# Performance work log

Hardware: AMD Instinct MI355X
Metric: run time of the kernel (lower is better)

The kernel has to match this reference:

```python
import jax, jax.numpy as jnp
import numpy as np

B, S, NT, D, NU = 1024, 200, 10000, 256, 100000
BETA_1 = 0.1


def setup_inputs() -> dict:
    key = jax.random.key(0)
    ks = jax.random.split(key, 6)
    user_id = jax.random.randint(ks[0], (B,), 0, NU)
    event_type = jax.random.randint(ks[1], (B, S), 0, NT + 1)  # 0 = pad
    adjacent_matrix = jax.random.uniform(ks[2], (NT, NT), dtype=jnp.float32)
    pop_encoding = jax.random.normal(ks[3], (NT + 1, D), dtype=jnp.float32)
    event_emb = jax.random.normal(ks[4], (NT + 1, D), dtype=jnp.float32) * 0.02
    user_emb = jax.random.normal(ks[5], (NU, D), dtype=jnp.float32) * 0.02
    return dict(user_id=user_id, event_type=event_type,
                adjacent_matrix=adjacent_matrix, pop_encoding=pop_encoding,
                evaluation=0, event_emb=event_emb, user_emb=user_emb)


def _l2norm(x, eps):
    # tf.nn.l2_normalize: x * rsqrt(max(sum(x^2), eps))
    return x * jax.lax.rsqrt(jnp.maximum(jnp.sum(x * x, axis=-1, keepdims=True), eps))


def reference(user_id, event_type, adjacent_matrix, pop_encoding, evaluation, event_emb, user_emb):
    non_pad = (event_type != 0).astype(jnp.float32)[..., None]          # [B,S,1]
    enc = event_emb[event_type]                                          # [B,S,D]
    usr = user_emb[user_id]                                              # [B,D]
    pop = pop_encoding[event_type] * non_pad                             # [B,S,D]
    # enc += sign(enc) * l2_normalize(user_output) (default eps 1e-12)
    enc = enc + jnp.sign(enc) * _l2norm(usr, 1e-12)[:, None, :]
    # per-sample adjacency: two-axis gather of the item-item matrix
    idx = jnp.where(event_type > 0, event_type - 1, 0)                   # [B,S]
    adj = adjacent_matrix[idx[:, :, None], idx[:, None, :]]              # [B,S,S]
    has_valid = (jnp.sum(event_type > 0, axis=1) > 0).astype(jnp.float32)
    adj = adj * has_valid[:, None, None]  # rows with all-pad stay zero, as in the loop
    output = jnp.mean(enc, axis=1)                                       # [B,D]
    user_embeddings = jnp.concatenate([output, jnp.mean(pop, axis=1) * BETA_1], axis=-1)  # [B,2D]
    if evaluation:
        item_encoding = event_emb[1:]                                    # [NT,D]
        scores = user_embeddings[:, :D] @ item_encoding.T
    else:
        item_encoding = jnp.concatenate([event_emb[1:], pop_encoding[1:] * BETA_1], axis=-1)  # [NT,2D]
        scores = user_embeddings @ item_encoding.T                       # [B,NT]
    prediction = jnp.tanh(_l2norm(scores, 1e-05))
    return prediction, user_embeddings, pop, adj
```

## Files before the change

### kernel.cpp

```cpp
#include <hip/hip_runtime.h>
#include <math.h>

#define NB 1024
#define NS 200
#define NTOK 10000
#define ND 256
#define BETA 0.1f

static constexpr size_t PRED_OFF = 0;
static constexpr size_t UE_OFF   = (size_t)NB * NTOK;
static constexpr size_t POP_OFF  = UE_OFF + (size_t)NB * 2 * ND;
static constexpr size_t ADJ_OFF  = POP_OFF + (size_t)NB * NS * ND;

static constexpr size_t WS_SIDX   = 0;
static constexpr size_t WS_HV     = WS_SIDX + (size_t)NB * NS;
static constexpr size_t WS_COUNTS = WS_HV + NB;
static constexpr size_t WS_OFFS   = WS_COUNTS + NTOK;
static constexpr size_t WS_CURSOR = WS_OFFS + NTOK + 1;
static constexpr size_t WS_PAIRS  = WS_CURSOR + NTOK;

__global__ __launch_bounds__(256) void k_embed(
    const int* __restrict__ user_id,
    const int* __restrict__ event_type,
    const float* __restrict__ pop_encoding,
    const float* __restrict__ event_emb,
    const float* __restrict__ user_emb,
    float* __restrict__ ue,
    float* __restrict__ pop)
{
    const int b = blockIdx.x;
    const int d = threadIdx.x;

    const int uid = user_id[b];
    const float u = user_emb[(size_t)uid * ND + d];

    float ss = u * u;
    #pragma unroll
    for (int o = 32; o > 0; o >>= 1) ss += __shfl_down(ss, o, 64);
    __shared__ float wss[4];
    const int wid = d >> 6, lane = d & 63;
    if (lane == 0) wss[wid] = ss;
    __syncthreads();
    const float tot = wss[0] + wss[1] + wss[2] + wss[3];
    const float nu = u * rsqrtf(fmaxf(tot, 1e-12f));

    __shared__ int et_s[NS];
    if (d < NS) et_s[d] = event_type[(size_t)b * NS + d];
    __syncthreads();

    float acc = 0.f, pacc = 0.f;
    #pragma unroll 4
    for (int s = 0; s < NS; ++s) {
        const int et = et_s[s];
        const float e = event_emb[(size_t)et * ND + d];
        const float sg = (e > 0.f) ? 1.f : ((e < 0.f) ? -1.f : 0.f);
        acc += e + sg * nu;
        float p = pop_encoding[(size_t)et * ND + d];
        p = (et != 0) ? p : 0.f;
        pacc += p;
        __builtin_nontemporal_store(p, &pop[((size_t)b * NS + s) * ND + d]);
    }
    ue[(size_t)b * (2 * ND) + d]      = acc * (1.f / NS);
    ue[(size_t)b * (2 * ND) + ND + d] = pacc * (1.f / NS) * BETA;
}

__global__ __launch_bounds__(256) void k_zero(int* __restrict__ counts)
{
    const int i = blockIdx.x * 256 + threadIdx.x;
    if (i < NTOK) counts[i] = 0;
}

__global__ __launch_bounds__(256) void k_prep(
    const int* __restrict__ event_type,
    int* __restrict__ sidx_all,
    float* __restrict__ hvf,
    int* __restrict__ counts)
{
    const int b = blockIdx.x;
    const int t = threadIdx.x;
    __shared__ int hv_s;
    if (t == 0) hv_s = 0;
    __syncthreads();
    if (t < NS) {
        const int et = event_type[(size_t)b * NS + t];
        const int r  = (et > 0) ? (et - 1) : 0;
        sidx_all[(size_t)b * NS + t] = r;
        if (et > 0) hv_s = 1;
        atomicAdd(&counts[r], 1);
    }
    __syncthreads();
    if (t == 0) hvf[b] = hv_s ? 1.f : 0.f;
}

#define SCAN_CHUNK 40
__global__ __launch_bounds__(256) void k_scan(
    const int* __restrict__ counts,
    int* __restrict__ offsets,
    int* __restrict__ cursor)
{
    const int t = threadIdx.x;
    int sum = 0;
    int local[SCAN_CHUNK];
    #pragma unroll
    for (int k = 0; k < SCAN_CHUNK; ++k) {
        const int idx = t * SCAN_CHUNK + k;
        const int c = (idx < NTOK) ? counts[idx] : 0;
        local[k] = c;
        sum += c;
    }
    __shared__ int part[256];
    part[t] = sum;
    __syncthreads();
    for (int o = 1; o < 256; o <<= 1) {
        const int v = (t >= o) ? part[t - o] : 0;
        __syncthreads();
        part[t] += v;
        __syncthreads();
    }
    int running = part[t] - sum;
    #pragma unroll
    for (int k = 0; k < SCAN_CHUNK; ++k) {
        const int idx = t * SCAN_CHUNK + k;
        if (idx < NTOK) {
            offsets[idx] = running;
            cursor[idx]  = running;
            running += local[k];
        }
    }
    if (t == 255) offsets[NTOK] = part[255];
}

__global__ __launch_bounds__(256) void k_scatter(
    const int* __restrict__ sidx_all,
    int* __restrict__ cursor,
    int* __restrict__ pairs)
{
    const int b = blockIdx.x;
    const int t = threadIdx.x;
    if (t < NS) {
        const int r = sidx_all[(size_t)b * NS + t];
        const int slot = atomicAdd(&cursor[r], 1);
        pairs[slot] = b * NS + t;
    }
}

__global__ __launch_bounds__(256) void k_adj2(
    const float* __restrict__ A,
    const int* __restrict__ sidx_all,
    const int* __restrict__ offsets,
    const int* __restrict__ pairs,
    const float* __restrict__ hvf,
    float* __restrict__ adj)
{
    const int r = blockIdx.x;
    const int t = threadIdx.x;
    const int p0 = offsets[r];
    const int n  = offsets[r + 1] - p0;
    if (n == 0) return;

    __shared__ __align__(16) float rowlds[NTOK];
    const float4* Arow = (const float4*)(A + (size_t)r * NTOK);
    #pragma unroll 4
    for (int l = t; l < NTOK / 4; l += 256)
        ((float4*)rowlds)[l] = Arow[l];
    __syncthreads();

    const int n_el = n * NS;
    for (int l = t; l < n_el; l += 256) {
        const int pi = l / NS;
        const int j  = l - pi * NS;
        const int pv = pairs[p0 + pi];
        const int b  = pv / NS;
        const int c  = sidx_all[(size_t)b * NS + j];
        const float v = rowlds[c] * hvf[b];
        __builtin_nontemporal_store(v, &adj[(size_t)pv * NS + j]);
    }
}

typedef __attribute__((ext_vector_type(8))) short bf16x8;
typedef __attribute__((ext_vector_type(4))) float f32x4;

static __device__ inline unsigned short f2bf(float f) {
    unsigned int u = __float_as_uint(f);
    return (unsigned short)((u + 0x7fffu + ((u >> 16) & 1u)) >> 16);
}

#define GBM 128
#define GBN 128
#define GBK 32
#define LDK 40

__global__ __launch_bounds__(256) void k_gemm_mfma(
    const float* __restrict__ ue,
    const float* __restrict__ event_emb,
    const float* __restrict__ pop_encoding,
    float* __restrict__ scores)
{
    __shared__ __align__(16) unsigned short As[GBM * LDK];
    __shared__ __align__(16) unsigned short Bs[GBN * LDK];

    const int t  = threadIdx.x;
    const int bn = blockIdx.x, bm = blockIdx.y;
    const int m0 = bm * GBM, n0 = bn * GBN;

    const int wave = t >> 6, lane = t & 63;
    const int ww = wave & 1, wm = wave >> 1;
    const int lr = lane & 15;
    const int kg = lane >> 4;

    const int kq = t & 7;
    const int rq = t >> 3;

    f32x4 acc[4][4] = {};

    for (int k0 = 0; k0 < 512; k0 += GBK) {
        #pragma unroll
        for (int i = 0; i < 4; ++i) {
            const int r = rq + 32 * i;
            const float4 v = *(const float4*)&ue[(size_t)(m0 + r) * 512 + k0 + kq * 4];
            ushort4 h;
            h.x = f2bf(v.x); h.y = f2bf(v.y); h.z = f2bf(v.z); h.w = f2bf(v.w);
            *(ushort4*)&As[r * LDK + kq * 4] = h;
        }
        const bool loK = (k0 < 256);
        const float scale = loK ? 1.f : BETA;
        #pragma unroll
        for (int i = 0; i < 4; ++i) {
            const int r = rq + 32 * i;
            const int gn = n0 + r;
            ushort4 h = {0, 0, 0, 0};
            if (gn < NTOK) {
                const float* src = loK
                    ? &event_emb[(size_t)(gn + 1) * ND + k0 + kq * 4]
                    : &pop_encoding[(size_t)(gn + 1) * ND + (k0 - 256) + kq * 4];
                const float4 v = *(const float4*)src;
                h.x = f2bf(v.x * scale); h.y = f2bf(v.y * scale);
                h.z = f2bf(v.z * scale); h.w = f2bf(v.w * scale);
            }
            *(ushort4*)&Bs[r * LDK + kq * 4] = h;
        }
        __syncthreads();

        bf16x8 a[4], b[4];
        #pragma unroll
        for (int mf = 0; mf < 4; ++mf)
            a[mf] = *(const bf16x8*)&As[(wm * 64 + mf * 16 + lr) * LDK + kg * 8];
        #pragma unroll
        for (int nf = 0; nf < 4; ++nf)
            b[nf] = *(const bf16x8*)&Bs[(ww * 64 + nf * 16 + lr) * LDK + kg * 8];
        #pragma unroll
        for (int mf = 0; mf < 4; ++mf)
            #pragma unroll
            for (int nf = 0; nf < 4; ++nf)
                acc[mf][nf] = __builtin_amdgcn_mfma_f32_16x16x32_bf16(
                    a[mf], b[nf], acc[mf][nf], 0, 0, 0);
        __syncthreads();
    }

    #pragma unroll
    for (int mf = 0; mf < 4; ++mf) {
        const int row = m0 + wm * 64 + mf * 16 + kg * 4;
        #pragma unroll
        for (int nf = 0; nf < 4; ++nf) {
            const int col = n0 + ww * 64 + nf * 16 + lr;
            if (col < NTOK) {
                #pragma unroll
                for (int r = 0; r < 4; ++r)
                    scores[(size_t)(row + r) * NTOK + col] = acc[mf][nf][r];
            }
        }
    }
}

__global__ __launch_bounds__(256) void k_norm(float* __restrict__ scores)
{
    const int b = blockIdx.x;
    const int t = threadIdx.x;
    float* row = scores + (size_t)b * NTOK;

    float ss = 0.f;
    for (int n = t; n < NTOK; n += 256) {
        const float v = row[n];
        ss += v * v;
    }
    #pragma unroll
    for (int o = 32; o > 0; o >>= 1) ss += __shfl_down(ss, o, 64);
    __shared__ float wss[4];
    const int wid = t >> 6, lane = t & 63;
    if (lane == 0) wss[wid] = ss;
    __syncthreads();
    const float tot = wss[0] + wss[1] + wss[2] + wss[3];
    const float rs = rsqrtf(fmaxf(tot, 1e-5f));

    for (int n = t; n < NTOK; n += 256)
        row[n] = tanhf(row[n] * rs);
}

extern "C" void kernel_launch(void* const* d_in, const int* in_sizes, int n_in,
                              void* d_out, int out_size, void* d_ws, size_t ws_size,
                              hipStream_t stream) {
    const int*   user_id      = (const int*)d_in[0];
    const int*   event_type   = (const int*)d_in[1];
    const float* adjacent     = (const float*)d_in[2];
    const float* pop_encoding = (const float*)d_in[3];
    const float* event_emb    = (const float*)d_in[5];
    const float* user_emb     = (const float*)d_in[6];

    float* out  = (float*)d_out;
    float* pred = out + PRED_OFF;
    float* ue   = out + UE_OFF;
    float* pop  = out + POP_OFF;
    float* adj  = out + ADJ_OFF;

    int*   ws       = (int*)d_ws;
    int*   sidx_all = ws + WS_SIDX;
    float* hvf      = (float*)(ws + WS_HV);
    int*   counts   = ws + WS_COUNTS;
    int*   offsets  = ws + WS_OFFS;
    int*   cursor   = ws + WS_CURSOR;
    int*   pairs    = ws + WS_PAIRS;

    k_embed<<<NB, 256, 0, stream>>>(user_id, event_type, pop_encoding,
                                    event_emb, user_emb, ue, pop);

    k_zero<<<(NTOK + 255) / 256, 256, 0, stream>>>(counts);
    k_prep<<<NB, 256, 0, stream>>>(event_type, sidx_all, hvf, counts);
    k_scan<<<1, 256, 0, stream>>>(counts, offsets, cursor);
    k_scatter<<<NB, 256, 0, stream>>>(sidx_all, cursor, pairs);
    k_adj2<<<NTOK, 256, 0, stream>>>(adjacent, sidx_all, offsets, pairs, hvf, adj);

    dim3 ggrid((NTOK + GBN - 1) / GBN, NB / GBM);
    k_gemm_mfma<<<ggrid, 256, 0, stream>>>(ue, event_emb, pop_encoding, pred);
    k_norm<<<NB, 256, 0, stream>>>(pred);
}
```

Baseline: 385.7 us.

## Pre-convert GEMM operands to bf16 and vectorize embed, adjacency and norm kernels

Adds a pass that converts the item encoding (event_emb and scaled pop_encoding) to a packed bf16 matrix, and has k_embed also write a bf16 copy of the user embeddings. The GEMM can then load bf16 directly, with no fp32 loads or in-loop conversion. k_embed is rewritten so that each wave handles a quarter of the sequence with float4 loads and stores, followed by a shared-memory reduction. k_adj2 assigns one pair per wave with int4/float4 vectorized gathers and stores, and k_norm uses float4 accesses. The cost is an extra kernel launch and extra workspace traffic for the bf16 copies.

```diff
diff --git a/kernel.cpp b/kernel.cpp
--- a/kernel.cpp
+++ b/kernel.cpp
@@ -18,6 +18,16 @@
 static constexpr size_t WS_OFFS   = WS_COUNTS + NTOK;
 static constexpr size_t WS_CURSOR = WS_OFFS + NTOK + 1;
 static constexpr size_t WS_PAIRS  = WS_CURSOR + NTOK;
+static constexpr size_t WS_UEBF   = 440640;
+static constexpr size_t WS_IEBF   = WS_UEBF + 262144;
+
+typedef __attribute__((ext_vector_type(8))) short bf16x8;
+typedef __attribute__((ext_vector_type(4))) float f32x4;
+
+static __device__ inline unsigned short f2bf(float f) {
+    unsigned int u = __float_as_uint(f);
+    return (unsigned short)((u + 0x7fffu + ((u >> 16) & 1u)) >> 16);
+}
 
 __global__ __launch_bounds__(256) void k_embed(
     const int* __restrict__ user_id,
@@ -26,42 +36,86 @@
     const float* __restrict__ event_emb,
     const float* __restrict__ user_emb,
     float* __restrict__ ue,
+    unsigned short* __restrict__ ue_bf,
     float* __restrict__ pop)
 {
-    const int b = blockIdx.x;
-    const int d = threadIdx.x;
+    const int b  = blockIdx.x;
+    const int t  = threadIdx.x;
+    const int sg = t >> 6;
+    const int tl = t & 63;
 
     const int uid = user_id[b];
-    const float u = user_emb[(size_t)uid * ND + d];
-
-    float ss = u * u;
-    #pragma unroll
-    for (int o = 32; o > 0; o >>= 1) ss += __shfl_down(ss, o, 64);
-    __shared__ float wss[4];
-    const int wid = d >> 6, lane = d & 63;
-    if (lane == 0) wss[wid] = ss;
-    __syncthreads();
-    const float tot = wss[0] + wss[1] + wss[2] + wss[3];
-    const float nu = u * rsqrtf(fmaxf(tot, 1e-12f));
+    const float4 u4 = *(const float4*)&user_emb[(size_t)uid * ND + tl * 4];
+
+    float ss = u4.x * u4.x + u4.y * u4.y + u4.z * u4.z + u4.w * u4.w;
+    #pragma unroll
+    for (int o = 32; o > 0; o >>= 1) ss += __shfl_xor(ss, o, 64);
+    const float rn = rsqrtf(fmaxf(ss, 1e-12f));
+    const float4 nu4 = {u4.x * rn, u4.y * rn, u4.z * rn, u4.w * rn};
 
     __shared__ int et_s[NS];
-    if (d < NS) et_s[d] = event_type[(size_t)b * NS + d];
-    __syncthreads();
-
-    float acc = 0.f, pacc = 0.f;
-    #pragma unroll 4
-    for (int s = 0; s < NS; ++s) {
+    if (t < NS) et_s[t] = event_type[(size_t)b * NS + t];
+    __syncthreads();
+
+    float4 eacc = {0.f, 0.f, 0.f, 0.f};
+    float4 pacc = {0.f, 0.f, 0.f, 0.f};
+    #pragma unroll 2
+    for (int it = 0; it < NS / 4; ++it) {
+        const int s  = sg + 4 * it;
         const int et = et_s[s];
-        const float e = event_emb[(size_t)et * ND + d];
-        const float sg = (e > 0.f) ? 1.f : ((e < 0.f) ? -1.f : 0.f);
-        acc += e + sg * nu;
-        float p = pop_encoding[(size_t)et * ND + d];
-        p = (et != 0) ? p : 0.f;
-        pacc += p;
-        __builtin_nontemporal_store(p, &pop[((size_t)b * NS + s) * ND + d]);
-    }
-    ue[(size_t)b * (2 * ND) + d]      = acc * (1.f / NS);
-    ue[(size_t)b * (2 * ND) + ND + d] = pacc * (1.f / NS) * BETA;
+        const float4 e = *(const float4*)&event_emb[(size_t)et * ND + tl * 4];
+        float4 p = *(const float4*)&pop_encoding[(size_t)et * ND + tl * 4];
+        const float z = (et != 0) ? 1.f : 0.f;
+        p.x *= z; p.y *= z; p.z *= z; p.w *= z;
+        eacc.x += e.x + ((e.x > 0.f) ? nu4.x : ((e.x < 0.f) ? -nu4.x : 0.f));
+        eacc.y += e.y + ((e.y > 0.f) ? nu4.y : ((e.y < 0.f) ? -nu4.y : 0.f));
+        eacc.z += e.z + ((e.z > 0.f) ? nu4.z : ((e.z < 0.f) ? -nu4.z : 0.f));
+        eacc.w += e.w + ((e.w > 0.f) ? nu4.w : ((e.w < 0.f) ? -nu4.w : 0.f));
+        pacc.x += p.x; pacc.y += p.y; pacc.z += p.z; pacc.w += p.w;
+        const f32x4 pv = {p.x, p.y, p.z, p.w};
+        __builtin_nontemporal_store(pv, (f32x4*)&pop[((size_t)b * NS + s) * ND + tl * 4]);
+    }
+
+    __shared__ __align__(16) float4 es[4][64];
+    __shared__ __align__(16) float4 ps[4][64];
+    es[sg][tl] = eacc;
+    ps[sg][tl] = pacc;
+    __syncthreads();
+
+    if (t < 64) {
+        float4 ef = es[0][t], pf = ps[0][t];
+        #pragma unroll
+        for (int w = 1; w < 4; ++w) {
+            const float4 e2 = es[w][t], p2 = ps[w][t];
+            ef.x += e2.x; ef.y += e2.y; ef.z += e2.z; ef.w += e2.w;
+            pf.x += p2.x; pf.y += p2.y; pf.z += p2.z; pf.w += p2.w;
+        }
+        const float se = 1.f / NS, sp = BETA / NS;
+        const float4 eo = {ef.x * se, ef.y * se, ef.z * se, ef.w * se};
+        const float4 po = {pf.x * sp, pf.y * sp, pf.z * sp, pf.w * sp};
+        *(float4*)&ue[(size_t)b * 512 + t * 4]       = eo;
+        *(float4*)&ue[(size_t)b * 512 + 256 + t * 4] = po;
+        ushort4 he = {f2bf(eo.x), f2bf(eo.y), f2bf(eo.z), f2bf(eo.w)};
+        ushort4 hp = {f2bf(po.x), f2bf(po.y), f2bf(po.z), f2bf(po.w)};
+        *(ushort4*)&ue_bf[(size_t)b * 512 + t * 4]       = he;
+        *(ushort4*)&ue_bf[(size_t)b * 512 + 256 + t * 4] = hp;
+    }
+}
+
+__global__ __launch_bounds__(256) void k_iebf(
+    const float* __restrict__ ee,
+    const float* __restrict__ pe,
+    unsigned short* __restrict__ ie)
+{
+    const int idx = blockIdx.x * 256 + threadIdx.x;
+    if (idx >= NTOK * 128) return;
+    const int row = idx >> 7;
+    const int kq  = idx & 127;
+    float4 v; float sc;
+    if (kq < 64) { v = *(const float4*)&ee[(size_t)(row + 1) * ND + kq * 4]; sc = 1.f; }
+    else         { v = *(const float4*)&pe[(size_t)(row + 1) * ND + (kq - 64) * 4]; sc = BETA; }
+    ushort4 h = {f2bf(v.x * sc), f2bf(v.y * sc), f2bf(v.z * sc), f2bf(v.w * sc)};
+    *(ushort4*)&ie[(size_t)row * 512 + kq * 4] = h;
 }
 
 __global__ __launch_bounds__(256) void k_zero(int* __restrict__ counts)
@@ -165,24 +219,21 @@
         ((float4*)rowlds)[l] = Arow[l];
     __syncthreads();
 
-    const int n_el = n * NS;
-    for (int l = t; l < n_el; l += 256) {
-        const int pi = l / NS;
-        const int j  = l - pi * NS;
+    const int wave = t >> 6, lane = t & 63;
+    for (int pi = wave; pi < n; pi += 4) {
         const int pv = pairs[p0 + pi];
         const int b  = pv / NS;
-        const int c  = sidx_all[(size_t)b * NS + j];
-        const float v = rowlds[c] * hvf[b];
-        __builtin_nontemporal_store(v, &adj[(size_t)pv * NS + j]);
-    }
-}
-
-typedef __attribute__((ext_vector_type(8))) short bf16x8;
-typedef __attribute__((ext_vector_type(4))) float f32x4;
-
-static __device__ inline unsigned short f2bf(float f) {
-    unsigned int u = __float_as_uint(f);
-    return (unsigned short)((u + 0x7fffu + ((u >> 16) & 1u)) >> 16);
+        const float hv = hvf[b];
+        if (lane < 50) {
+            const int4 c4 = *(const int4*)&sidx_all[(size_t)b * NS + lane * 4];
+            f32x4 v;
+            v.x = rowlds[c4.x] * hv;
+            v.y = rowlds[c4.y] * hv;
+            v.z = rowlds[c4.z] * hv;
+            v.w = rowlds[c4.w] * hv;
+            __builtin_nontemporal_store(v, (f32x4*)&adj[(size_t)pv * NS + lane * 4]);
+        }
+    }
 }
 
 #define GBM 128
@@ -191,9 +242,8 @@
 #define LDK 40
 
 __global__ __launch_bounds__(256) void k_gemm_mfma(
-    const float* __restrict__ ue,
-    const float* __restrict__ event_emb,
-    const float* __restrict__ pop_encoding,
+    const unsigned short* __restrict__ ue_bf,
+    const unsigned short* __restrict__ ie_bf,
     float* __restrict__ scores)
 {
     __shared__ __align__(16) unsigned short As[GBM * LDK];
@@ -217,26 +267,16 @@
         #pragma unroll
         for (int i = 0; i < 4; ++i) {
             const int r = rq + 32 * i;
-            const float4 v = *(const float4*)&ue[(size_t)(m0 + r) * 512 + k0 + kq * 4];
-            ushort4 h;
-            h.x = f2bf(v.x); h.y = f2bf(v.y); h.z = f2bf(v.z); h.w = f2bf(v.w);
-            *(ushort4*)&As[r * LDK + kq * 4] = h;
-        }
-        const bool loK = (k0 < 256);
-        const float scale = loK ? 1.f : BETA;
+            *(ushort4*)&As[r * LDK + kq * 4] =
+                *(const ushort4*)&ue_bf[(size_t)(m0 + r) * 512 + k0 + kq * 4];
+        }
         #pragma unroll
         for (int i = 0; i < 4; ++i) {
             const int r = rq + 32 * i;
             const int gn = n0 + r;
             ushort4 h = {0, 0, 0, 0};
-            if (gn < NTOK) {
-                const float* src = loK
-                    ? &event_emb[(size_t)(gn + 1) * ND + k0 + kq * 4]
-                    : &pop_encoding[(size_t)(gn + 1) * ND + (k0 - 256) + kq * 4];
-                const float4 v = *(const float4*)src;
-                h.x = f2bf(v.x * scale); h.y = f2bf(v.y * scale);
-                h.z = f2bf(v.z * scale); h.w = f2bf(v.w * scale);
-            }
+            if (gn < NTOK)
+                h = *(const ushort4*)&ie_bf[(size_t)gn * 512 + k0 + kq * 4];
             *(ushort4*)&Bs[r * LDK + kq * 4] = h;
         }
         __syncthreads();
@@ -276,12 +316,12 @@
 {
     const int b = blockIdx.x;
     const int t = threadIdx.x;
-    float* row = scores + (size_t)b * NTOK;
+    float4* row4 = (float4*)(scores + (size_t)b * NTOK);
 
     float ss = 0.f;
-    for (int n = t; n < NTOK; n += 256) {
-        const float v = row[n];
-        ss += v * v;
+    for (int l = t; l < NTOK / 4; l += 256) {
+        const float4 v = row4[l];
+        ss += v.x * v.x + v.y * v.y + v.z * v.z + v.w * v.w;
     }
     #pragma unroll
     for (int o = 32; o > 0; o >>= 1) ss += __shfl_down(ss, o, 64);
@@ -292,8 +332,12 @@
     const float tot = wss[0] + wss[1] + wss[2] + wss[3];
     const float rs = rsqrtf(fmaxf(tot, 1e-5f));
 
-    for (int n = t; n < NTOK; n += 256)
-        row[n] = tanhf(row[n] * rs);
+    for (int l = t; l < NTOK / 4; l += 256) {
+        float4 v = row4[l];
+        v.x = tanhf(v.x * rs); v.y = tanhf(v.y * rs);
+        v.z = tanhf(v.z * rs); v.w = tanhf(v.w * rs);
+        row4[l] = v;
+    }
 }
 
 extern "C" void kernel_launch(void* const* d_in, const int* in_sizes, int n_in,
@@ -319,9 +363,12 @@
     int*   offsets  = ws + WS_OFFS;
     int*   cursor   = ws + WS_CURSOR;
     int*   pairs    = ws + WS_PAIRS;
+    unsigned short* ue_bf = (unsigned short*)(ws + WS_UEBF);
+    unsigned short* ie_bf = (unsigned short*)(ws + WS_IEBF);
 
     k_embed<<<NB, 256, 0, stream>>>(user_id, event_type, pop_encoding,
-                                    event_emb, user_emb, ue, pop);
+                                    event_emb, user_emb, ue, ue_bf, pop);
+    k_iebf<<<(NTOK * 128 + 255) / 256, 256, 0, stream>>>(event_emb, pop_encoding, ie_bf);
 
     k_zero<<<(NTOK + 255) / 256, 256, 0, stream>>>(counts);
     k_prep<<<NB, 256, 0, stream>>>(event_type, sidx_all, hvf, counts);
@@ -330,6 +377,6 @@
     k_adj2<<<NTOK, 256, 0, stream>>>(adjacent, sidx_all, offsets, pairs, hvf, adj);
 
     dim3 ggrid((NTOK + GBN - 1) / GBN, NB / GBM);
-    k_gemm_mfma<<<ggrid, 256, 0, stream>>>(ue, event_emb, pop_encoding, pred);
+    k_gemm_mfma<<<ggrid, 256, 0, stream>>>(ue_bf, ie_bf, pred);
     k_norm<<<NB, 256, 0, stream>>>(pred);
 }
```

After: 319.8 us. -17.1%, faster.
